# Performance work log

Measured on AMD Instinct MI355X. Metric: run time of the kernel, lower is better.

## Reference

```python
import jax, jax.numpy as jnp
import numpy as np

# 4D conv dimension numbers: N=batch, C/I/O=channels, T,Z,Y,X = 4 spatial dims
DN = ('NCTZYX', 'OITZYX', 'NCTZYX')
PAD = [(1, 1)] * 4  # padding=1 on each of the 4 spatial dims


def setup_inputs() -> dict:
    key = jax.random.key(0)
    kx, kw = jax.random.split(key)
    B, Cin, Cout = 1, 16, 4
    T, D, H, Wd = 10, 32, 64, 64
    K = 3
    x = jax.random.normal(kx, (B, Cin, T, D, H, Wd), dtype=jnp.float32)
    # xavier_uniform over [Cout, Cin, 3,3,3,3]
    fan_in = Cin * K ** 4
    fan_out = Cout * K ** 4
    limit = float(np.sqrt(6.0 / (fan_in + fan_out)))
    W = jax.random.uniform(kw, (Cout, Cin, K, K, K, K), dtype=jnp.float32,
                           minval=-limit, maxval=limit)
    b = jnp.zeros((Cout,), dtype=jnp.float32)
    return {"x": x, "W": W, "b": b}


def reference(x, W, b):
    # True 4D convolution (stride 1, padding 1, 'same' output) + channel softmax
    y = jax.lax.conv_general_dilated(
        x, W,
        window_strides=(1, 1, 1, 1),
        padding=PAD,
        dimension_numbers=DN,
    )
    y = y + b[None, :, None, None, None, None]
    return jax.nn.softmax(y, axis=1)
```

## Files before the change

kernel.cpp:

```cpp
#include <hip/hip_runtime.h>
#include <hip/hip_bf16.h>

#define CIN  16
#define COUT 4
#define TT   10
#define ZZ   32
#define YY   64
#define XX   64

constexpr int SX_CI = TT * ZZ * YY * XX;
constexpr int SX_T  = ZZ * YY * XX;
constexpr int SX_Z  = YY * XX;
constexpr int WCO   = CIN * 81;

constexpr int XT_TB = ZZ * YY * XX * CIN * 2;
constexpr int XT_ZB = YY * XX * CIN * 2;
constexpr int XT_YB = XX * CIN * 2;
constexpr size_t XT_BYTES = (size_t)TT * XT_TB;
constexpr size_t BTAB     = XT_BYTES;
constexpr size_t ZOFF     = BTAB + 9 * 2048;
constexpr size_t WS_NEED  = ZOFF + 2048;

typedef short  short8 __attribute__((ext_vector_type(8)));
typedef float  f32x4  __attribute__((ext_vector_type(4)));

__device__ __forceinline__ unsigned short f2bf(float f) {
    union { __hip_bfloat16 h; unsigned short u; } c;
    c.h = __float2bfloat16(f);
    return c.u;
}
__device__ __forceinline__ unsigned int pk(float a, float b) {
    return (unsigned int)f2bf(a) | ((unsigned int)f2bf(b) << 16);
}

#define TXS 36
#define TYS (64 * TXS)
__global__ __launch_bounds__(256) void transpose_x(const float* __restrict__ x,
                                                   char* __restrict__ ws) {
    __shared__ char lds[16 * TYS];
    const int lane = threadIdx.x & 63;
    const int w    = threadIdx.x >> 6;
    const int yq = blockIdx.x, z = blockIdx.y, t = blockIdx.z;
    const int y0 = yq * 16;
    const int rl = w * 4 + (lane >> 4);
    const int x0 = (lane & 15) * 4;
    const size_t gbase = (size_t)t * SX_T + (size_t)z * SX_Z +
                         (size_t)(y0 + rl) * XX + x0;
#pragma unroll
    for (int cp = 0; cp < 8; ++cp) {
        const float4 f0 = *(const float4*)(x + (size_t)(2 * cp + 0) * SX_CI + gbase);
        const float4 f1 = *(const float4*)(x + (size_t)(2 * cp + 1) * SX_CI + gbase);
        char* p = lds + rl * TYS + x0 * TXS + cp * 4;
        *(unsigned int*)(p + 0 * TXS) = pk(f0.x, f1.x);
        *(unsigned int*)(p + 1 * TXS) = pk(f0.y, f1.y);
        *(unsigned int*)(p + 2 * TXS) = pk(f0.z, f1.z);
        *(unsigned int*)(p + 3 * TXS) = pk(f0.w, f1.w);
    }
    __syncthreads();
#pragma unroll
    for (int s = 0; s < 4; ++s) {
        const int r2 = w * 4 + s;
        char* rowp = ws + (((size_t)t * ZZ + z) * YY + (y0 + r2)) * 2048;
#pragma unroll
        for (int half = 0; half < 2; ++half) {
            const int c = half * 64 + lane;
            const uint4 d = *(const uint4*)(lds + r2 * TYS + (c >> 1) * TXS +
                                            (c & 1) * 16);
            *(uint4*)(rowp + c * 16) = d;
        }
    }
}

__global__ void prep_B(const float* __restrict__ W, char* __restrict__ ws) {
    const int g = blockIdx.x * 256 + threadIdx.x;
    if (g < 1152) {
        const int p = g >> 7, rem = g & 127, frag = rem >> 6, L = rem & 63;
        const int q = L >> 4, n = L & 15, co = n & 3, dx = n >> 2;
        const int dt = p / 3, dz = p % 3;
        unsigned int d[4];
#pragma unroll
        for (int j = 0; j < 4; ++j) {
            float v0 = 0.f, v1 = 0.f;
            if (dx < 3) {
                if (frag == 0) {
                    const int dy = q >> 1;
                    const int ci0 = (q & 1) * 8 + 2 * j;
                    v0 = W[(co * CIN + ci0) * 81 + dt * 27 + dz * 9 + dy * 3 + dx];
                    v1 = W[(co * CIN + ci0 + 1) * 81 + dt * 27 + dz * 9 + dy * 3 + dx];
                } else if (q < 2) {
                    const int ci0 = q * 8 + 2 * j;
                    v0 = W[(co * CIN + ci0) * 81 + dt * 27 + dz * 9 + 6 + dx];
                    v1 = W[(co * CIN + ci0 + 1) * 81 + dt * 27 + dz * 9 + 6 + dx];
                }
            }
            d[j] = pk(v0, v1);
        }
        *(uint4*)(ws + BTAB + (size_t)p * 2048 + frag * 1024 + (size_t)L * 16) =
            make_uint4(d[0], d[1], d[2], d[3]);
    } else if (g < 1280) {
        *(uint4*)(ws + ZOFF + (size_t)(g - 1152) * 16) = make_uint4(0, 0, 0, 0);
    }
}

#define GL16(SRC, DST) __builtin_amdgcn_global_load_lds( \
    (const __attribute__((address_space(1))) unsigned int*)(SRC), \
    (__attribute__((address_space(3))) unsigned int*)(DST), 16, 0, 0)

#define LROW 21
__global__ __launch_bounds__(256, 2) void conv_mfma(
        const char* __restrict__ ws,
        const float* __restrict__ bias,
        float* __restrict__ out) {
    __shared__ char smem[2 * 18 * 2048];
    const int lane = threadIdx.x;
    const int wid  = __builtin_amdgcn_readfirstlane(threadIdx.y);
    const int bid = blockIdx.x;
    const int xcd = bid & 7, lid = bid >> 3;
    const int z0 = 4 * xcd + (lid & 3);
    const int yq = (lid >> 2) & 3;
    const int t0 = lid >> 4;
    const int y0 = yq * 16;
    const int m = lane & 15, q = lane >> 4, h = q & 1, dyA = q >> 1;
    const int e2 = 2 * m + h;
    const int wid4 = wid * 4;

    f32x4 acc[4][4];
#pragma unroll
    for (int r = 0; r < 4; ++r)
#pragma unroll
        for (int xt = 0; xt < 4; ++xt) acc[r][xt] = (f32x4){0.f, 0.f, 0.f, 0.f};

#define STAGE(P, BUF) { \
    const int dtS = (P) / 3, dzS = (P) % 3; \
    const int t_in = t0 + dtS - 1, z_in = z0 + dzS - 1; \
    const bool pv = ((unsigned)t_in < TT) && ((unsigned)z_in < ZZ); \
    const int pbase = pv ? (t_in * XT_TB + z_in * XT_ZB) : 0; \
    _Pragma("unroll") \
    for (int k = 0; k < 9; ++k) { \
        const int rw = (wid + 4 * k) >> 1; \
        const int hf = ((wid + 4 * k) & 1) * 1024; \
        const int y_in = y0 - 1 + rw; \
        const bool rv = pv && ((unsigned)y_in < YY); \
        const char* srcS = ws + (rv ? (size_t)(pbase + y_in * XT_YB) : ZOFF) \
                              + hf + lane * 16; \
        GL16(srcS, smem + (BUF) * 36864 + rw * 2048 + hf + lane * 16); \
    } }

#define COMPUTE(P, BUF) { \
    const char* bbC = smem + (BUF) * 36864; \
    const short8 BfA = *(const short8*)(ws + BTAB + (P) * 2048 + lane * 16); \
    const short8 BfB = *(const short8*)(ws + BTAB + (P) * 2048 + 1024 + lane * 16); \
    _Pragma("unroll") \
    for (int xt = 0; xt < 4; ++xt) { \
        const int sw = (32 * xt + e2) * 16; \
        const char* colp = bbC + wid4 * 2048 + sw; \
        short8 Rw0 = *(const short8*)(colp + 0 * 2048); \
        short8 Rw1 = *(const short8*)(colp + 1 * 2048); \
        short8 Rw2 = *(const short8*)(colp + 2 * 2048); \
        short8 Rw3 = *(const short8*)(colp + 3 * 2048); \
        short8 Rw4 = *(const short8*)(colp + 4 * 2048); \
        short8 Rw5 = *(const short8*)(colp + 5 * 2048); \
        const short8 fa0 = dyA ? Rw1 : Rw0; \
        const short8 fa1 = dyA ? Rw2 : Rw1; \
        const short8 fa2 = dyA ? Rw3 : Rw2; \
        const short8 fa3 = dyA ? Rw4 : Rw3; \
        acc[0][xt] = __builtin_amdgcn_mfma_f32_16x16x32_bf16(fa0, BfA, acc[0][xt], 0, 0, 0); \
        acc[0][xt] = __builtin_amdgcn_mfma_f32_16x16x32_bf16(Rw2, BfB, acc[0][xt], 0, 0, 0); \
        acc[1][xt] = __builtin_amdgcn_mfma_f32_16x16x32_bf16(fa1, BfA, acc[1][xt], 0, 0, 0); \
        acc[1][xt] = __builtin_amdgcn_mfma_f32_16x16x32_bf16(Rw3, BfB, acc[1][xt], 0, 0, 0); \
        acc[2][xt] = __builtin_amdgcn_mfma_f32_16x16x32_bf16(fa2, BfA, acc[2][xt], 0, 0, 0); \
        acc[2][xt] = __builtin_amdgcn_mfma_f32_16x16x32_bf16(Rw4, BfB, acc[2][xt], 0, 0, 0); \
        acc[3][xt] = __builtin_amdgcn_mfma_f32_16x16x32_bf16(fa3, BfA, acc[3][xt], 0, 0, 0); \
        acc[3][xt] = __builtin_amdgcn_mfma_f32_16x16x32_bf16(Rw5, BfB, acc[3][xt], 0, 0, 0); \
    } }

    STAGE(0, 0) __syncthreads();
    STAGE(1, 1) COMPUTE(0, 0) __syncthreads();
    STAGE(2, 0) COMPUTE(1, 1) __syncthreads();
    STAGE(3, 1) COMPUTE(2, 0) __syncthreads();
    STAGE(4, 0) COMPUTE(3, 1) __syncthreads();
    STAGE(5, 1) COMPUTE(4, 0) __syncthreads();
    STAGE(6, 0) COMPUTE(5, 1) __syncthreads();
    STAGE(7, 1) COMPUTE(6, 0) __syncthreads();
    STAGE(8, 0) COMPUTE(7, 1) __syncthreads();
    COMPUTE(8, 0) __syncthreads();
#undef STAGE
#undef COMPUTE

    const float bi0 = bias[0], bi1 = bias[1], bi2 = bias[2], bi3 = bias[3];
    float* swave = (float*)smem + wid * (66 * LROW);
    if (lane < LROW) {
        swave[lane] = 0.f;
        swave[65 * LROW + lane] = 0.f;
    }
    const int colw = lane & 15;
    const int rowq = (lane >> 4) * 4 + 1;
#pragma unroll
    for (int r = 0; r < 4; ++r) {
#pragma unroll
        for (int xt = 0; xt < 4; ++xt)
#pragma unroll
            for (int reg = 0; reg < 4; ++reg)
                swave[(xt * 16 + rowq + reg) * LROW + colw] = acc[r][xt][reg];
        float lg0 = bi0, lg1 = bi1, lg2 = bi2, lg3 = bi3;
#pragma unroll
        for (int dx = 0; dx < 3; ++dx) {
            const float* sp = swave + (lane + dx) * LROW + dx * 4;
            lg0 += sp[0]; lg1 += sp[1]; lg2 += sp[2]; lg3 += sp[3];
        }
        const float mx = fmaxf(fmaxf(lg0, lg1), fmaxf(lg2, lg3));
        const float e0 = __expf(lg0 - mx);
        const float e1 = __expf(lg1 - mx);
        const float e2v = __expf(lg2 - mx);
        const float e3 = __expf(lg3 - mx);
        const float inv = 1.f / (e0 + e1 + e2v + e3);
        const int y = y0 + wid4 + r;
        float* op = out + (size_t)t0 * SX_T + (size_t)z0 * SX_Z + (size_t)y * XX + lane;
        op[0 * (size_t)SX_CI] = e0 * inv;
        op[1 * (size_t)SX_CI] = e1 * inv;
        op[2 * (size_t)SX_CI] = e2v * inv;
        op[3 * (size_t)SX_CI] = e3 * inv;
    }
}

__global__ __launch_bounds__(256, 4) void conv4d_softmax_vec(
        const float* __restrict__ x, const float* __restrict__ W,
        const float* __restrict__ b, float* __restrict__ out) {
    const int lane = threadIdx.x;
    const int xg = lane & 15, yl = lane >> 4;
    const int y = blockIdx.x * 16 + threadIdx.y * 4 + yl;
    const int z0 = blockIdx.y, t0 = blockIdx.z, x0 = xg * 4;
    float acc[COUT][4];
#pragma unroll
    for (int c = 0; c < COUT; ++c)
#pragma unroll
        for (int xi = 0; xi < 4; ++xi) acc[c][xi] = 0.f;
    for (int ci = 0; ci < CIN; ++ci) {
        const float* xc = x + (size_t)ci * SX_CI;
        const float* wc = W + ci * 81;
#pragma unroll
        for (int dt = 0; dt < 3; ++dt) {
            const int t_in = t0 + dt - 1;
            const int t_c = min(max(t_in, 0), TT - 1);
            const bool tv = (unsigned)t_in < TT;
#pragma unroll
            for (int dz = 0; dz < 3; ++dz) {
                const int z_in = z0 + dz - 1;
                const int z_c = min(max(z_in, 0), ZZ - 1);
                const bool tzvv = tv && ((unsigned)z_in < ZZ);
                const float* plane = xc + (size_t)t_c * SX_T + (size_t)z_c * SX_Z;
                const float* wb = wc + (dt * 3 + dz) * 9;
#pragma unroll
                for (int e = 0; e < 3; ++e) {
                    const int y_in = y + e - 1;
                    const int y_c = min(max(y_in, 0), YY - 1);
                    const bool v = tzvv && ((unsigned)y_in < YY);
                    float4 f = *(const float4*)(plane + y_c * XX + x0);
                    f.x = v ? f.x : 0.f; f.y = v ? f.y : 0.f;
                    f.z = v ? f.z : 0.f; f.w = v ? f.w : 0.f;
                    float hl = __shfl(f.w, (lane - 1) & 63, 64);
                    hl = (xg == 0) ? 0.f : hl;
                    float hr = __shfl(f.x, (lane + 1) & 63, 64);
                    hr = (xg == 15) ? 0.f : hr;
                    const float win[6] = {hl, f.x, f.y, f.z, f.w, hr};
#pragma unroll
                    for (int co = 0; co < COUT; ++co) {
                        const float* wp = wb + co * WCO + e * 3;
                        const float w0 = wp[0], w1 = wp[1], w2 = wp[2];
#pragma unroll
                        for (int xi = 0; xi < 4; ++xi) {
                            float a = acc[co][xi];
                            a = fmaf(win[xi], w0, a);
                            a = fmaf(win[xi + 1], w1, a);
                            a = fmaf(win[xi + 2], w2, a);
                            acc[co][xi] = a;
                        }
                    }
                }
            }
        }
    }
    const float b0 = b[0], b1 = b[1], b2 = b[2], b3 = b[3];
    float4 rr[COUT];
#pragma unroll
    for (int xi = 0; xi < 4; ++xi) {
        const float a0 = acc[0][xi] + b0, a1 = acc[1][xi] + b1;
        const float a2 = acc[2][xi] + b2, a3 = acc[3][xi] + b3;
        const float mm = fmaxf(fmaxf(a0, a1), fmaxf(a2, a3));
        const float e0 = __expf(a0 - mm), e1 = __expf(a1 - mm);
        const float e2 = __expf(a2 - mm), e3 = __expf(a3 - mm);
        const float inv = 1.f / (e0 + e1 + e2 + e3);
        ((float*)&rr[0])[xi] = e0 * inv; ((float*)&rr[1])[xi] = e1 * inv;
        ((float*)&rr[2])[xi] = e2 * inv; ((float*)&rr[3])[xi] = e3 * inv;
    }
    float* op = out + (size_t)t0 * SX_T + (size_t)z0 * SX_Z + (size_t)y * XX + x0;
#pragma unroll
    for (int co = 0; co < COUT; ++co)
        *(float4*)(op + (size_t)co * SX_CI) = rr[co];
}

extern "C" void kernel_launch(void* const* d_in, const int* in_sizes, int n_in,
                              void* d_out, int out_size, void* d_ws, size_t ws_size,
                              hipStream_t stream) {
    const float* x = (const float*)d_in[0];
    const float* W = (const float*)d_in[1];
    const float* b = (const float*)d_in[2];
    float* out = (float*)d_out;

    if (ws_size >= WS_NEED) {
        char* ws = (char*)d_ws;
        transpose_x<<<dim3(4, ZZ, TT), dim3(256), 0, stream>>>(x, ws);
        prep_B<<<dim3(5), dim3(256), 0, stream>>>(W, ws);
        conv_mfma<<<dim3(1280), dim3(64, 4), 0, stream>>>(ws, b, out);
    } else {
        conv4d_softmax_vec<<<dim3(4, ZZ, TT), dim3(64, 4), 0, stream>>>(x, W, b, out);
    }
}
```

Measured before the change: 172.1 us.

## Retile conv_mfma to 2 z-planes by 8 rows for plane reuse and occupancy

Changes each block's output tile from 1 z-plane by 16 y-rows to 2 z-planes by 8 y-rows. Each staged input (t,z) plane now feeds both output z-planes, giving 12 stages instead of 9 per two z outputs. This cuts redundant input-plane loads along z. It also halves LDS per block and raises launch bounds to 4 blocks per CU, trading per-block work and an extra pipeline stage for higher occupancy and less global traffic.

```diff
diff --git a/kernel.cpp b/kernel.cpp
--- a/kernel.cpp
+++ b/kernel.cpp
@@ -107,83 +107,94 @@
     (__attribute__((address_space(3))) unsigned int*)(DST), 16, 0, 0)
 
 #define LROW 21
-__global__ __launch_bounds__(256, 2) void conv_mfma(
+__global__ __launch_bounds__(256, 4) void conv_mfma(
         const char* __restrict__ ws,
         const float* __restrict__ bias,
         float* __restrict__ out) {
-    __shared__ char smem[2 * 18 * 2048];
+    __shared__ char smem[2 * 10 * 2048];
     const int lane = threadIdx.x;
     const int wid  = __builtin_amdgcn_readfirstlane(threadIdx.y);
     const int bid = blockIdx.x;
     const int xcd = bid & 7, lid = bid >> 3;
-    const int z0 = 4 * xcd + (lid & 3);
-    const int yq = (lid >> 2) & 3;
+    const int z0 = 4 * xcd + 2 * (lid & 1);
+    const int yq = (lid >> 1) & 7;
     const int t0 = lid >> 4;
-    const int y0 = yq * 16;
+    const int y0 = yq * 8;
     const int m = lane & 15, q = lane >> 4, h = q & 1, dyA = q >> 1;
     const int e2 = 2 * m + h;
-    const int wid4 = wid * 4;
-
-    f32x4 acc[4][4];
-#pragma unroll
-    for (int r = 0; r < 4; ++r)
-#pragma unroll
-        for (int xt = 0; xt < 4; ++xt) acc[r][xt] = (f32x4){0.f, 0.f, 0.f, 0.f};
+    const int wid2 = wid * 2;
+
+    f32x4 acc[2][2][4];
+#pragma unroll
+    for (int z = 0; z < 2; ++z)
+#pragma unroll
+        for (int r = 0; r < 2; ++r)
+#pragma unroll
+            for (int xt = 0; xt < 4; ++xt) acc[z][r][xt] = (f32x4){0.f, 0.f, 0.f, 0.f};
 
 #define STAGE(P, BUF) { \
-    const int dtS = (P) / 3, dzS = (P) % 3; \
-    const int t_in = t0 + dtS - 1, z_in = z0 + dzS - 1; \
+    constexpr int dtS = (P) >> 2, jS = (P) & 3; \
+    const int t_in = t0 + dtS - 1, z_in = z0 + jS - 1; \
     const bool pv = ((unsigned)t_in < TT) && ((unsigned)z_in < ZZ); \
     const int pbase = pv ? (t_in * XT_TB + z_in * XT_ZB) : 0; \
     _Pragma("unroll") \
-    for (int k = 0; k < 9; ++k) { \
-        const int rw = (wid + 4 * k) >> 1; \
-        const int hf = ((wid + 4 * k) & 1) * 1024; \
+    for (int k = 0; k < 5; ++k) { \
+        const int idx = wid + 4 * k; \
+        const int rw = idx >> 1; \
+        const int hf = (idx & 1) * 1024; \
         const int y_in = y0 - 1 + rw; \
         const bool rv = pv && ((unsigned)y_in < YY); \
         const char* srcS = ws + (rv ? (size_t)(pbase + y_in * XT_YB) : ZOFF) \
                               + hf + lane * 16; \
-        GL16(srcS, smem + (BUF) * 36864 + rw * 2048 + hf + lane * 16); \
+        GL16(srcS, smem + (BUF) * 20480 + rw * 2048 + hf + lane * 16); \
     } }
 
 #define COMPUTE(P, BUF) { \
-    const char* bbC = smem + (BUF) * 36864; \
-    const short8 BfA = *(const short8*)(ws + BTAB + (P) * 2048 + lane * 16); \
-    const short8 BfB = *(const short8*)(ws + BTAB + (P) * 2048 + 1024 + lane * 16); \
+    constexpr int dtC = (P) >> 2, jC = (P) & 3; \
+    constexpr int paC = dtC * 3 + (jC <= 2 ? jC : 0); \
+    constexpr int pbC = dtC * 3 + (jC >= 1 ? jC - 1 : 0); \
+    const char* bbC = smem + (BUF) * 20480; \
+    const short8 BfAa = *(const short8*)(ws + BTAB + paC * 2048 + lane * 16); \
+    const short8 BfBa = *(const short8*)(ws + BTAB + paC * 2048 + 1024 + lane * 16); \
+    const short8 BfAb = *(const short8*)(ws + BTAB + pbC * 2048 + lane * 16); \
+    const short8 BfBb = *(const short8*)(ws + BTAB + pbC * 2048 + 1024 + lane * 16); \
     _Pragma("unroll") \
     for (int xt = 0; xt < 4; ++xt) { \
         const int sw = (32 * xt + e2) * 16; \
-        const char* colp = bbC + wid4 * 2048 + sw; \
-        short8 Rw0 = *(const short8*)(colp + 0 * 2048); \
-        short8 Rw1 = *(const short8*)(colp + 1 * 2048); \
-        short8 Rw2 = *(const short8*)(colp + 2 * 2048); \
-        short8 Rw3 = *(const short8*)(colp + 3 * 2048); \
-        short8 Rw4 = *(const short8*)(colp + 4 * 2048); \
-        short8 Rw5 = *(const short8*)(colp + 5 * 2048); \
+        const char* colp = bbC + wid2 * 2048 + sw; \
+        const short8 Rw0 = *(const short8*)(colp + 0 * 2048); \
+        const short8 Rw1 = *(const short8*)(colp + 1 * 2048); \
+        const short8 Rw2 = *(const short8*)(colp + 2 * 2048); \
+        const short8 Rw3 = *(const short8*)(colp + 3 * 2048); \
         const short8 fa0 = dyA ? Rw1 : Rw0; \
         const short8 fa1 = dyA ? Rw2 : Rw1; \
-        const short8 fa2 = dyA ? Rw3 : Rw2; \
-        const short8 fa3 = dyA ? Rw4 : Rw3; \
-        acc[0][xt] = __builtin_amdgcn_mfma_f32_16x16x32_bf16(fa0, BfA, acc[0][xt], 0, 0, 0); \
-        acc[0][xt] = __builtin_amdgcn_mfma_f32_16x16x32_bf16(Rw2, BfB, acc[0][xt], 0, 0, 0); \
-        acc[1][xt] = __builtin_amdgcn_mfma_f32_16x16x32_bf16(fa1, BfA, acc[1][xt], 0, 0, 0); \
-        acc[1][xt] = __builtin_amdgcn_mfma_f32_16x16x32_bf16(Rw3, BfB, acc[1][xt], 0, 0, 0); \
-        acc[2][xt] = __builtin_amdgcn_mfma_f32_16x16x32_bf16(fa2, BfA, acc[2][xt], 0, 0, 0); \
-        acc[2][xt] = __builtin_amdgcn_mfma_f32_16x16x32_bf16(Rw4, BfB, acc[2][xt], 0, 0, 0); \
-        acc[3][xt] = __builtin_amdgcn_mfma_f32_16x16x32_bf16(fa3, BfA, acc[3][xt], 0, 0, 0); \
-        acc[3][xt] = __builtin_amdgcn_mfma_f32_16x16x32_bf16(Rw5, BfB, acc[3][xt], 0, 0, 0); \
+        if (jC <= 2) { \
+            acc[0][0][xt] = __builtin_amdgcn_mfma_f32_16x16x32_bf16(fa0, BfAa, acc[0][0][xt], 0, 0, 0); \
+            acc[0][0][xt] = __builtin_amdgcn_mfma_f32_16x16x32_bf16(Rw2, BfBa, acc[0][0][xt], 0, 0, 0); \
+            acc[0][1][xt] = __builtin_amdgcn_mfma_f32_16x16x32_bf16(fa1, BfAa, acc[0][1][xt], 0, 0, 0); \
+            acc[0][1][xt] = __builtin_amdgcn_mfma_f32_16x16x32_bf16(Rw3, BfBa, acc[0][1][xt], 0, 0, 0); \
+        } \
+        if (jC >= 1) { \
+            acc[1][0][xt] = __builtin_amdgcn_mfma_f32_16x16x32_bf16(fa0, BfAb, acc[1][0][xt], 0, 0, 0); \
+            acc[1][0][xt] = __builtin_amdgcn_mfma_f32_16x16x32_bf16(Rw2, BfBb, acc[1][0][xt], 0, 0, 0); \
+            acc[1][1][xt] = __builtin_amdgcn_mfma_f32_16x16x32_bf16(fa1, BfAb, acc[1][1][xt], 0, 0, 0); \
+            acc[1][1][xt] = __builtin_amdgcn_mfma_f32_16x16x32_bf16(Rw3, BfBb, acc[1][1][xt], 0, 0, 0); \
+        } \
     } }
 
-    STAGE(0, 0) __syncthreads();
-    STAGE(1, 1) COMPUTE(0, 0) __syncthreads();
-    STAGE(2, 0) COMPUTE(1, 1) __syncthreads();
-    STAGE(3, 1) COMPUTE(2, 0) __syncthreads();
-    STAGE(4, 0) COMPUTE(3, 1) __syncthreads();
-    STAGE(5, 1) COMPUTE(4, 0) __syncthreads();
-    STAGE(6, 0) COMPUTE(5, 1) __syncthreads();
-    STAGE(7, 1) COMPUTE(6, 0) __syncthreads();
-    STAGE(8, 0) COMPUTE(7, 1) __syncthreads();
-    COMPUTE(8, 0) __syncthreads();
+    STAGE(0, 0)  __syncthreads();
+    STAGE(1, 1)  COMPUTE(0, 0)  __syncthreads();
+    STAGE(2, 0)  COMPUTE(1, 1)  __syncthreads();
+    STAGE(3, 1)  COMPUTE(2, 0)  __syncthreads();
+    STAGE(4, 0)  COMPUTE(3, 1)  __syncthreads();
+    STAGE(5, 1)  COMPUTE(4, 0)  __syncthreads();
+    STAGE(6, 0)  COMPUTE(5, 1)  __syncthreads();
+    STAGE(7, 1)  COMPUTE(6, 0)  __syncthreads();
+    STAGE(8, 0)  COMPUTE(7, 1)  __syncthreads();
+    STAGE(9, 1)  COMPUTE(8, 0)  __syncthreads();
+    STAGE(10, 0) COMPUTE(9, 1)  __syncthreads();
+    STAGE(11, 1) COMPUTE(10, 0) __syncthreads();
+    COMPUTE(11, 1) __syncthreads();
 #undef STAGE
 #undef COMPUTE
 
@@ -196,30 +207,34 @@
     const int colw = lane & 15;
     const int rowq = (lane >> 4) * 4 + 1;
 #pragma unroll
-    for (int r = 0; r < 4; ++r) {
-#pragma unroll
-        for (int xt = 0; xt < 4; ++xt)
-#pragma unroll
-            for (int reg = 0; reg < 4; ++reg)
-                swave[(xt * 16 + rowq + reg) * LROW + colw] = acc[r][xt][reg];
-        float lg0 = bi0, lg1 = bi1, lg2 = bi2, lg3 = bi3;
-#pragma unroll
-        for (int dx = 0; dx < 3; ++dx) {
-            const float* sp = swave + (lane + dx) * LROW + dx * 4;
-            lg0 += sp[0]; lg1 += sp[1]; lg2 += sp[2]; lg3 += sp[3];
+    for (int z = 0; z < 2; ++z) {
+#pragma unroll
+        for (int r = 0; r < 2; ++r) {
+#pragma unroll
+            for (int xt = 0; xt < 4; ++xt)
+#pragma unroll
+                for (int reg = 0; reg < 4; ++reg)
+                    swave[(xt * 16 + rowq + reg) * LROW + colw] = acc[z][r][xt][reg];
+            float lg0 = bi0, lg1 = bi1, lg2 = bi2, lg3 = bi3;
+#pragma unroll
+            for (int dx = 0; dx < 3; ++dx) {
+                const float* sp = swave + (lane + dx) * LROW + dx * 4;
+                lg0 += sp[0]; lg1 += sp[1]; lg2 += sp[2]; lg3 += sp[3];
+            }
+            const float mx = fmaxf(fmaxf(lg0, lg1), fmaxf(lg2, lg3));
+            const float e0 = __expf(lg0 - mx);
+            const float e1 = __expf(lg1 - mx);
+            const float e2v = __expf(lg2 - mx);
+            const float e3 = __expf(lg3 - mx);
+            const float inv = 1.f / (e0 + e1 + e2v + e3);
+            const int y = y0 + wid2 + r;
+            float* op = out + (size_t)t0 * SX_T + (size_t)(z0 + z) * SX_Z +
+                        (size_t)y * XX + lane;
+            op[0 * (size_t)SX_CI] = e0 * inv;
+            op[1 * (size_t)SX_CI] = e1 * inv;
+            op[2 * (size_t)SX_CI] = e2v * inv;
+            op[3 * (size_t)SX_CI] = e3 * inv;
         }
-        const float mx = fmaxf(fmaxf(lg0, lg1), fmaxf(lg2, lg3));
-        const float e0 = __expf(lg0 - mx);
-        const float e1 = __expf(lg1 - mx);
-        const float e2v = __expf(lg2 - mx);
-        const float e3 = __expf(lg3 - mx);
-        const float inv = 1.f / (e0 + e1 + e2v + e3);
-        const int y = y0 + wid4 + r;
-        float* op = out + (size_t)t0 * SX_T + (size_t)z0 * SX_Z + (size_t)y * XX + lane;
-        op[0 * (size_t)SX_CI] = e0 * inv;
-        op[1 * (size_t)SX_CI] = e1 * inv;
-        op[2 * (size_t)SX_CI] = e2v * inv;
-        op[3 * (size_t)SX_CI] = e3 * inv;
     }
 }
 
```

Measured after the change: 164.5 us. 1.05x faster.
